# Kernel tuning notes

Hardware: AMD Instinct MI355X
Metric: run time of the kernel (lower is better)

Reference implementation:

```python
import jax, jax.numpy as jnp
import numpy as np

N_BINS = 10
THRESHOLD = 0.5
FOR_NEG_CLASS = False


def reference(outputs, labels):
    """Single-pass equivalent of CalibrationCurve.update starting from zeroed buffers.

    Returns jnp.stack([prob_sum, tp_sum, count]) of shape (3, N_BINS).
    Bin b covers (low[b], high[b]] with edges = linspace(-1e-6, 1, N_BINS+1),
    exactly matching the torch per-bin masked reductions, fused into one
    bucketize + three segment-sums (one HBM pass instead of 3*N_BINS).
    """
    if FOR_NEG_CLASS:
        outputs = 1.0 - outputs
        labels = 1.0 - labels
    edges = jnp.linspace(jnp.float32(-1e-6), jnp.float32(1.0), N_BINS + 1)
    high = edges[1:]   # upper bound per bin (inclusive)
    low0 = edges[0]    # global lower bound (exclusive)

    x = outputs.ravel()
    y = labels.ravel()
    # smallest b with x <= high[b]  (side='left': high[b-1] < x <= high[b])
    bin_idx = jnp.searchsorted(high, x, side='left')
    valid = (x > low0) & (x <= high[-1])
    # invalid elements get index N_BINS -> dropped by segment_sum (out of range)
    idx = jnp.where(valid, bin_idx, N_BINS)

    prob_sum = jax.ops.segment_sum(x, idx, num_segments=N_BINS)
    tp_sum = jax.ops.segment_sum((y > THRESHOLD).astype(jnp.float32), idx, num_segments=N_BINS)
    count = jax.ops.segment_sum(jnp.ones_like(x), idx, num_segments=N_BINS)
    return jnp.stack([prob_sum, tp_sum, count])  # (3, N_BINS)


def setup_inputs() -> dict:
    key = jax.random.key(0)
    k1, k2 = jax.random.split(key)
    outputs = jax.random.uniform(k1, (32, 1024, 1024), dtype=jnp.float32)
    labels = jax.random.uniform(k2, (32, 1024, 1024), dtype=jnp.float32)
    return {"outputs": outputs, "labels": labels}
```

## Files before the change

kernel.cpp:

```cpp
#include <hip/hip_runtime.h>

#define NBINS 10
#define PART_STRIDE 32

__global__ __launch_bounds__(256) void calib_hist(
    const float* __restrict__ outputs,
    const float* __restrict__ labels,
    float* __restrict__ partials,
    long n)
{
    const int tid = threadIdx.x;
    const float low0 = -1e-6f;
    const float step = (1.0f - low0) / 10.0f;

    float        pacc[NBINS];
    unsigned int cacc[NBINS];
#pragma unroll
    for (int j = 0; j < NBINS; ++j) { pacc[j] = 0.0f; cacc[j] = 0u; }

    const long total4 = n >> 2;
    const float4* o4 = (const float4*)outputs;
    const float4* l4 = (const float4*)labels;
    const long gid = (long)blockIdx.x * blockDim.x + tid;
    const long gsz = (long)gridDim.x * blockDim.x;

    long i = gid;
    if (i < total4) {
        float4 o = o4[i];
        float4 l = l4[i];
        for (;;) {
            const long nexti = i + gsz;
            const bool have_next = (nexti < total4);
            float4 no, nl;
            if (have_next) { no = o4[nexti]; nl = l4[nexti]; }

            float xs[4] = {o.x, o.y, o.z, o.w};
            float ys[4] = {l.x, l.y, l.z, l.w};
#pragma unroll
            for (int k = 0; k < 4; ++k) {
                float x = xs[k];
                bool valid = (x > low0) & (x <= 1.0f);
                int e = (int)(x * 10.0f);
                e = e < 0 ? 0 : (e > 9 ? 9 : e);
                float fe  = (float)e;
                float hb0 = fmaf(fe,        step, low0);
                float hb1 = fmaf(fe + 1.0f, step, low0);
                int b = e + ((x > hb1) ? 1 : 0) - (((e > 0) & (x <= hb0)) ? 1 : 0);
                b = b < 0 ? 0 : (b > 9 ? 9 : b);
                b = valid ? b : NBINS;
                unsigned int pc = (ys[k] > 0.5f) ? 0x10001u : 1u;
#pragma unroll
                for (int j = 0; j < NBINS; ++j) {
                    bool hit = (b == j);
                    pacc[j] += hit ? x : 0.0f;
                    cacc[j] += hit ? pc : 0u;
                }
            }

            if (!have_next) break;
            o = no; l = nl; i = nexti;
        }
    }

    const long tail0 = total4 << 2;
    for (long t = tail0 + gid; t < n; t += gsz) {
        float x = outputs[t];
        float y = labels [t];
        bool valid = (x > low0) & (x <= 1.0f);
        int e = (int)(x * 10.0f);
        e = e < 0 ? 0 : (e > 9 ? 9 : e);
        float fe  = (float)e;
        float hb0 = fmaf(fe,        step, low0);
        float hb1 = fmaf(fe + 1.0f, step, low0);
        int b = e + ((x > hb1) ? 1 : 0) - (((e > 0) & (x <= hb0)) ? 1 : 0);
        b = b < 0 ? 0 : (b > 9 ? 9 : b);
        b = valid ? b : NBINS;
        unsigned int pc = (y > 0.5f) ? 0x10001u : 1u;
#pragma unroll
        for (int j = 0; j < NBINS; ++j) {
            bool hit = (b == j);
            pacc[j] += hit ? x : 0.0f;
            cacc[j] += hit ? pc : 0u;
        }
    }

    __shared__ float s_red[4][32];
    const int lane = tid & 63;
    const int wave = tid >> 6;
#pragma unroll
    for (int j = 0; j < NBINS; ++j) {
        float p  = pacc[j];
        float tp = (float)(cacc[j] >> 16);
        float ct = (float)(cacc[j] & 0xFFFFu);
#pragma unroll
        for (int off = 32; off > 0; off >>= 1) {
            p  += __shfl_xor(p,  off, 64);
            tp += __shfl_xor(tp, off, 64);
            ct += __shfl_xor(ct, off, 64);
        }
        if (lane == 0) {
            s_red[wave][j]             = p;
            s_red[wave][NBINS + j]     = tp;
            s_red[wave][2 * NBINS + j] = ct;
        }
    }
    __syncthreads();
    if (tid < 3 * NBINS) {
        float s = s_red[0][tid] + s_red[1][tid] + s_red[2][tid] + s_red[3][tid];
        partials[(long)blockIdx.x * PART_STRIDE + tid] = s;
    }
}

__global__ __launch_bounds__(256) void calib_reduce(
    const float* __restrict__ partials, float* __restrict__ out, int nrows)
{
    const int s   = blockIdx.x;
    const int tid = threadIdx.x;
    double acc = 0.0;
    for (int r = tid; r < nrows; r += 256)
        acc += (double)partials[(long)r * PART_STRIDE + s];
#pragma unroll
    for (int off = 32; off > 0; off >>= 1)
        acc += __shfl_down(acc, off, 64);
    __shared__ double wsum[4];
    if ((tid & 63) == 0) wsum[tid >> 6] = acc;
    __syncthreads();
    if (tid == 0) out[s] = (float)(wsum[0] + wsum[1] + wsum[2] + wsum[3]);
}

extern "C" void kernel_launch(void* const* d_in, const int* in_sizes, int n_in,
                              void* d_out, int out_size, void* d_ws, size_t ws_size,
                              hipStream_t stream) {
    const float* outputs = (const float*)d_in[0];
    const float* labels  = (const float*)d_in[1];
    float* out = (float*)d_out;
    long n = (long)in_sizes[0];

    int nblocks = 2048;
    size_t need = (size_t)nblocks * PART_STRIDE * sizeof(float);
    if (ws_size < need) {
        nblocks = (int)(ws_size / (PART_STRIDE * sizeof(float)));
        if (nblocks < 1) nblocks = 1;
    }
    float* partials = (float*)d_ws;

    calib_hist  <<<nblocks, 256, 0, stream>>>(outputs, labels, partials, n);
    calib_reduce<<<3 * NBINS, 256, 0, stream>>>(partials, out, nblocks);
}
```

Measured before the change: 289.2 us.

## Replace per-thread register bin accumulators with replicated LDS atomic histograms

```diff
diff --git a/kernel.cpp b/kernel.cpp
--- a/kernel.cpp
+++ b/kernel.cpp
@@ -1,6 +1,8 @@
 #include <hip/hip_runtime.h>
 
 #define NBINS 10
+#define NREP  8
+#define REPW  20
 #define PART_STRIDE 32
 
 __global__ __launch_bounds__(256) void calib_hist(
@@ -9,14 +11,17 @@
     float* __restrict__ partials,
     long n)
 {
+    __shared__ __align__(16) unsigned int s_hist[NREP * REPW];
+
     const int tid = threadIdx.x;
+    for (int j = tid; j < NREP * REPW; j += 256) s_hist[j] = 0u;
+    __syncthreads();
+
     const float low0 = -1e-6f;
     const float step = (1.0f - low0) / 10.0f;
 
-    float        pacc[NBINS];
-    unsigned int cacc[NBINS];
-#pragma unroll
-    for (int j = 0; j < NBINS; ++j) { pacc[j] = 0.0f; cacc[j] = 0u; }
+    unsigned int* __restrict__ rep  = &s_hist[(tid & (NREP - 1)) * REPW];
+    float*        __restrict__ repf = (float*)rep;
 
     const long total4 = n >> 2;
     const float4* o4 = (const float4*)outputs;
@@ -47,14 +52,12 @@
                 float hb1 = fmaf(fe + 1.0f, step, low0);
                 int b = e + ((x > hb1) ? 1 : 0) - (((e > 0) & (x <= hb0)) ? 1 : 0);
                 b = b < 0 ? 0 : (b > 9 ? 9 : b);
-                b = valid ? b : NBINS;
-                unsigned int pc = (ys[k] > 0.5f) ? 0x10001u : 1u;
-#pragma unroll
-                for (int j = 0; j < NBINS; ++j) {
-                    bool hit = (b == j);
-                    pacc[j] += hit ? x : 0.0f;
-                    cacc[j] += hit ? pc : 0u;
-                }
+                float        px = valid ? x : 0.0f;
+                unsigned int pc = valid ? ((ys[k] > 0.5f) ? 0x10001u : 1u) : 0u;
+                __hip_atomic_fetch_add(&repf[2 * b], px,
+                                       __ATOMIC_RELAXED, __HIP_MEMORY_SCOPE_WORKGROUP);
+                __hip_atomic_fetch_add(&rep[2 * b + 1], pc,
+                                       __ATOMIC_RELAXED, __HIP_MEMORY_SCOPE_WORKGROUP);
             }
 
             if (!have_next) break;
@@ -74,39 +77,28 @@
         float hb1 = fmaf(fe + 1.0f, step, low0);
         int b = e + ((x > hb1) ? 1 : 0) - (((e > 0) & (x <= hb0)) ? 1 : 0);
         b = b < 0 ? 0 : (b > 9 ? 9 : b);
-        b = valid ? b : NBINS;
-        unsigned int pc = (y > 0.5f) ? 0x10001u : 1u;
-#pragma unroll
-        for (int j = 0; j < NBINS; ++j) {
-            bool hit = (b == j);
-            pacc[j] += hit ? x : 0.0f;
-            cacc[j] += hit ? pc : 0u;
-        }
+        float        px = valid ? x : 0.0f;
+        unsigned int pc = valid ? ((y > 0.5f) ? 0x10001u : 1u) : 0u;
+        __hip_atomic_fetch_add(&repf[2 * b], px,
+                               __ATOMIC_RELAXED, __HIP_MEMORY_SCOPE_WORKGROUP);
+        __hip_atomic_fetch_add(&rep[2 * b + 1], pc,
+                               __ATOMIC_RELAXED, __HIP_MEMORY_SCOPE_WORKGROUP);
     }
 
-    __shared__ float s_red[4][32];
-    const int lane = tid & 63;
-    const int wave = tid >> 6;
+    __syncthreads();
+
+    if (tid < 3 * NBINS) {
+        const int b = tid % NBINS;
+        float s = 0.0f;
 #pragma unroll
-    for (int j = 0; j < NBINS; ++j) {
-        float p  = pacc[j];
-        float tp = (float)(cacc[j] >> 16);
-        float ct = (float)(cacc[j] & 0xFFFFu);
-#pragma unroll
-        for (int off = 32; off > 0; off >>= 1) {
-            p  += __shfl_xor(p,  off, 64);
-            tp += __shfl_xor(tp, off, 64);
-            ct += __shfl_xor(ct, off, 64);
+        for (int r = 0; r < NREP; ++r) {
+            if (tid < NBINS) {
+                s += ((float*)s_hist)[r * REPW + 2 * b];
+            } else {
+                unsigned int c = s_hist[r * REPW + 2 * b + 1];
+                s += (tid < 2 * NBINS) ? (float)(c >> 16) : (float)(c & 0xFFFFu);
+            }
         }
-        if (lane == 0) {
-            s_red[wave][j]             = p;
-            s_red[wave][NBINS + j]     = tp;
-            s_red[wave][2 * NBINS + j] = ct;
-        }
-    }
-    __syncthreads();
-    if (tid < 3 * NBINS) {
-        float s = s_red[0][tid] + s_red[1][tid] + s_red[2][tid] + s_red[3][tid];
         partials[(long)blockIdx.x * PART_STRIDE + tid] = s;
     }
 }
```

Result: slower. 366.2 us (+26.6%).
